# Kernel optimization log

Measured on AMD Instinct MI355X. Metric: run time of the kernel, lower is better.

## Reference

```python
import jax, jax.numpy as jnp
import numpy as np

# ---- constants from the source module ----
NB = [[0,1,2,3],[0,1,4],[0,2,5],[0,3,6],[1,4,7],[2,5,8],[3,6,9],[4,7,10],[5,8,11],[6,9],[7,10],[8,11],[12,13,14,15],[12,13,16],[12,14,17],[12,15],[13,16,18],[14,17,19],[16,18,20],[17,19,21],[18,20,22],[19,21,23],[20,22],[21,23]]
PARENT = np.array([0,0,0,0,1,2,3,4,5,6,7,8,9,9,9,12,13,14,16,17,18,19,20,21])  # root parent sentinel handled separately
KJ, NV, PREG = 24, 6890, 200
LEN = np.array([len(n) for n in NB])
NBR_IDX = np.zeros((KJ,4), np.int32)
NBR_VALID = np.zeros((KJ,4), np.float32)
for k, n in enumerate(NB):
    NBR_IDX[k,:len(n)] = n; NBR_VALID[k,:len(n)] = 1.0
BETA_POS = np.zeros((KJ,17), np.float32); BETA_POS[np.arange(KJ), 4*LEN] = 1.0
SLICE_MASK = np.zeros((23,17), np.float32)
for j in range(23):
    SLICE_MASK[j,:4*LEN[j]+1] = 1.0  # self.K[j] has 4*len(NB[j])+1 rows
NBR_IDX = jnp.asarray(NBR_IDX); NBR_VALID = jnp.asarray(NBR_VALID)
BETA_POS = jnp.asarray(BETA_POS); SLICE_MASK = jnpp = jnp.asarray(SLICE_MASK)


def setup_inputs() -> dict:
    key = jax.random.key(0)
    ks = jax.random.split(key, 9)
    V = jax.random.normal(ks[0], (PREG, NV, 3), jnp.float32)
    T = jax.random.normal(ks[1], (PREG, NV, 3), jnp.float32)
    J = jax.random.normal(ks[2], (PREG, KJ, 3), jnp.float32)
    theta = 0.3 * jax.random.normal(ks[3], (PREG, 72), jnp.float32)
    W_prime = jax.random.uniform(ks[4], (NV, KJ), jnp.float32)
    W_i = jax.random.uniform(ks[5], (NV, KJ), jnp.float32)
    W_i = W_i / W_i.sum(axis=1, keepdims=True)
    A = jax.random.uniform(ks[6], (23, NV), jnp.float32)
    K_mats = 0.01 * jax.random.normal(ks[7], (23, 17, 3 * NV), jnp.float32)
    K_mats = K_mats * SLICE_MASK[:, :, None]  # zero rows beyond the ragged per-joint size
    beta_2 = jnp.ones((1,), jnp.float32)
    return {"V": V, "T": T, "J": J, "theta": theta, "W_prime": W_prime, "W_i": W_i, "A": A, "K_mats": K_mats, "beta_2": beta_2, "epoch": 1}


def _rodrigues(pose):  # pose: (K,3)
    angle = jnp.maximum(jnp.linalg.norm(pose, axis=1, keepdims=True), 1e-8)
    axis = pose / angle
    x, y, z = axis[:, 0], axis[:, 1], axis[:, 2]
    zero = jnp.zeros_like(x)
    skew = jnp.stack([zero, -z, y, z, zero, -x, -y, x, zero], axis=1).reshape(-1, 3, 3)
    outer = axis[:, :, None] * axis[:, None, :]
    c = jnp.cos(angle)[:, :, None]
    s = jnp.sin(angle)[:, :, None]
    eye = jnp.eye(3, dtype=pose.dtype)[None]
    return c * eye + (1.0 - c) * outer + s * skew


def _compute_G(pose72, Jp):  # pose72: (72,), Jp: (K,3) -> (K,4,4)
    R = _rodrigues(pose72.reshape(KJ, 3))
    t = Jp - jnp.concatenate([jnp.zeros((1, 3), Jp.dtype), Jp[PARENT[1:]]], axis=0)
    G_local = jnp.zeros((KJ, 4, 4), Jp.dtype)
    G_local = G_local.at[:, :3, :3].set(R).at[:, :3, 3].set(t).at[:, 3, 3].set(1.0)
    Gs = [G_local[0]]
    for i in range(1, KJ):  # fixed 24-joint kinematic tree
        Gs.append(Gs[PARENT[i]] @ G_local[i])
    G = jnp.stack(Gs, axis=0)
    off = jnp.einsum('kij,kj->ki', G[:, :3, :3], Jp)  # homogeneous w=0 -> rotation only
    return G.at[:, :3, 3].add(-off)


def _axis2quat(p):  # (M,3) -> (M,4)
    angle = jnp.sqrt(jnp.maximum(jnp.sum(p ** 2, axis=1), 1e-16))
    n = p / angle[:, None]
    s = jnp.sin(angle / 2)
    return jnp.stack([n[:, 0] * s, n[:, 1] * s, n[:, 2] * s, jnp.cos(angle / 2) - 1.0], axis=1)


def reference(V, T, J, theta, W_prime, W_i, A, K_mats, beta_2, epoch):
    P = V.shape[0]
    b2 = beta_2[0]
    # normalized skinning weights
    W_relu = jax.nn.relu(W_prime)
    W_change = W_relu / (W_relu.sum(axis=1, keepdims=True) + 1e-8)
    # per-pose global joint transforms
    G_prime = jax.vmap(_compute_G)(theta, J)  # (P,K,4,4)
    # quaternion features and blend-shape correction
    q = _axis2quat(theta.reshape(P * KJ, 3)).reshape(P, KJ, 4)
    qg = q[:, NBR_IDX, :] * NBR_VALID[None, :, :, None]       # (P,K,4,4) neighbor gather
    q17 = jnp.concatenate([qg.reshape(P, KJ, 16), jnp.zeros((P, KJ, 1), q.dtype)], axis=-1)
    q17 = q17 + BETA_POS[None] * b2                            # beta_2 at column 4*len
    qm = q17[:, 1:, :] * SLICE_MASK[None]                      # ragged slice q_ne[:, j+1, :lenK]
    contrib = jnp.einsum('pjl,jlm->pjm', qm, K_mats).reshape(P, 23, NV, 3)
    T_p = jnp.einsum('pjnc,jn->pnc', contrib, jax.nn.relu(A)) + T
    # linear blend skinning
    T_h = jnp.concatenate([T_p, jnp.ones((P, NV, 1), T_p.dtype)], axis=-1)
    transformed = jnp.einsum('pkij,pnj->pnki', G_prime[:, :, :3, :], T_h)  # (P,N,K,3)
    verts = jnp.einsum('nk,pnkc->pnc', W_change, transformed)
    # energies
    e = float(epoch)
    g_wi = 0.1 * np.exp(-0.1 * e)
    g_w = 0.002 * np.exp(-0.008 * e)
    g_a = 0.001 * np.exp(-0.008 * e)
    g_k = 0.1 * np.exp(-0.008 * e)
    E_D = jnp.sum((V - verts) ** 2)
    E_Wi = jnp.sum((W_change - W_i) ** 2)
    E_W = jnp.sum(jnp.abs(W_change))
    E_A = jnp.sum(jnp.abs(A))
    E_K = jnp.sum(jnp.sqrt(jnp.sum(K_mats ** 2, axis=(1, 2))))
    E = E_D + g_wi * E_Wi + g_w * E_W + g_a * E_A + g_k * E_K
    return (E, verts)
```

## Files before the change

### kernel.cpp

```cpp
#include <hip/hip_runtime.h>
#include <math.h>

#define KJ 24
#define NV 6890
#define PREG 200
#define M_TOT (NV*3)
#define KDIM 391
#define KPAD 416
#define TP_STRIDE 20672
#define NMT64 323
#define NSTAGE (NMT64*13)
#define NMT32 646

#define EDP_OFF 0
#define EKP_OFF 5400
#define WIP_OFF 101984
#define EWP_OFF 102016
#define EAP_OFF 102048
#define RED_OFF 102080
#define G_OFF   102112
#define TP_OFF  159712
#define QBH_OFF_U 10903488
#define QBL_OFF_U 11009984
#define BTH_OFF_U 11116480
#define BTL_OFF_U 19716032
#define TP2_OFF 14157792

typedef __attribute__((ext_vector_type(8))) short short8;
typedef __attribute__((ext_vector_type(4))) float f32x4;
typedef __attribute__((ext_vector_type(4))) unsigned int u32x4;

__constant__ int c_PARENT[24] = {0,0,0,0,1,2,3,4,5,6,7,8,9,9,9,12,13,14,16,17,18,19,20,21};
__constant__ int c_DEPTH[24]  = {0,1,1,1,2,2,2,3,3,3,4,4,4,4,4,5,5,5,6,6,7,7,8,8};
__constant__ int c_LEN[24]    = {4,3,3,3,3,3,3,3,3,2,2,2,4,3,3,2,3,3,3,3,3,3,2,2};
__constant__ int c_NBR[24][4] = {
  {0,1,2,3},{0,1,4,0},{0,2,5,0},{0,3,6,0},{1,4,7,0},{2,5,8,0},{3,6,9,0},{4,7,10,0},
  {5,8,11,0},{6,9,0,0},{7,10,0,0},{8,11,0,0},{12,13,14,15},{12,13,16,0},{12,14,17,0},
  {12,15,0,0},{13,16,18,0},{14,17,19,0},{16,18,20,0},{17,19,21,0},{18,20,22,0},
  {19,21,23,0},{20,22,0,0},{21,23,0,0}};

__device__ __forceinline__ float waveReduce(float v) {
  #pragma unroll
  for (int off = 32; off > 0; off >>= 1) v += __shfl_down(v, off, 64);
  return v;
}
__device__ __forceinline__ unsigned short f2bf(float x) {
  union { float f; unsigned u; } v; v.f = x;
  unsigned r = v.u + 0x7FFFu + ((v.u >> 16) & 1u);
  return (unsigned short)(r >> 16);
}
__device__ __forceinline__ float bf2f(unsigned short h) {
  union { unsigned u; float f; } v; v.u = ((unsigned)h) << 16; return v.f;
}

__global__ __launch_bounds__(256) void kPre(const float* __restrict__ J,
                                            const float* __restrict__ theta,
                                            const float* __restrict__ beta2,
                                            const float* __restrict__ Wp,
                                            const float* __restrict__ Wi,
                                            const float* __restrict__ A,
                                            const float* __restrict__ K,
                                            float* __restrict__ ws) {
  unsigned short* qbh = (unsigned short*)ws + QBH_OFF_U;
  unsigned short* qbl = (unsigned short*)ws + QBL_OFF_U;
  int b = blockIdx.x;
  if (b < 50) {
    __shared__ float Gl[4][24][12];
    __shared__ float Gg[4][24][12];
    __shared__ float q[4][24][4];
    int w = threadIdx.x >> 6, t = threadIdx.x & 63;
    int p = b*4 + w;
    if (t < 24) {
      float x = theta[p*72 + 3*t + 0];
      float y = theta[p*72 + 3*t + 1];
      float z = theta[p*72 + 3*t + 2];
      float n2 = x*x + y*y + z*z;
      float ang = fmaxf(sqrtf(n2), 1e-8f);
      float ia = 1.f/ang;
      float ax = x*ia, ay = y*ia, az = z*ia;
      float c = cosf(ang), s = sinf(ang), C = 1.f - c;
      float jx = J[p*72+3*t], jy = J[p*72+3*t+1], jz = J[p*72+3*t+2];
      float tx = jx, ty = jy, tz = jz;
      if (t > 0) {
        int par = c_PARENT[t];
        tx -= J[p*72+3*par]; ty -= J[p*72+3*par+1]; tz -= J[p*72+3*par+2];
      }
      Gl[w][t][0]=c+C*ax*ax;   Gl[w][t][1]=C*ax*ay-s*az; Gl[w][t][2]=C*ax*az+s*ay; Gl[w][t][3]=tx;
      Gl[w][t][4]=C*ax*ay+s*az;Gl[w][t][5]=c+C*ay*ay;    Gl[w][t][6]=C*ay*az-s*ax; Gl[w][t][7]=ty;
      Gl[w][t][8]=C*ax*az-s*ay;Gl[w][t][9]=C*ay*az+s*ax; Gl[w][t][10]=c+C*az*az;   Gl[w][t][11]=tz;
      float ang2 = sqrtf(fmaxf(n2, 1e-16f));
      float inv2 = 1.f/ang2;
      float s2 = sinf(0.5f*ang2);
      q[w][t][0] = x*inv2*s2; q[w][t][1] = y*inv2*s2; q[w][t][2] = z*inv2*s2;
      q[w][t][3] = cosf(0.5f*ang2) - 1.f;
    }
    __syncthreads();
    for (int lev = 0; lev <= 8; lev++) {
      if (t < 24 && c_DEPTH[t] == lev) {
        if (lev == 0) {
          for (int i2 = 0; i2 < 12; i2++) Gg[w][0][i2] = Gl[w][0][i2];
        } else {
          int par = c_PARENT[t];
          for (int r = 0; r < 3; r++) {
            float g0 = Gg[w][par][r*4+0], g1 = Gg[w][par][r*4+1];
            float g2 = Gg[w][par][r*4+2], g3 = Gg[w][par][r*4+3];
            for (int c2 = 0; c2 < 4; c2++) {
              float v = g0*Gl[w][t][0+c2] + g1*Gl[w][t][4+c2] + g2*Gl[w][t][8+c2];
              if (c2 == 3) v += g3;
              Gg[w][t][r*4+c2] = v;
            }
          }
        }
      }
      __syncthreads();
    }
    if (t < 24) {
      float jx = J[p*72+3*t], jy = J[p*72+3*t+1], jz = J[p*72+3*t+2];
      float* gp = ws + G_OFF + p*288 + t*12;
      #pragma unroll
      for (int r = 0; r < 3; r++) {
        float off = Gg[w][t][r*4+0]*jx + Gg[w][t][r*4+1]*jy + Gg[w][t][r*4+2]*jz;
        Gg[w][t][r*4+3] -= off;
      }
      #pragma unroll
      for (int i2 = 0; i2 < 12; i2++) gp[i2] = Gg[w][t][i2];
    }
    __syncthreads();
    float b2 = beta2[0];
    for (int e = t; e < KDIM; e += 64) {
      int j = e / 17, l = e - 17*j;
      int k = j + 1;
      float val = 0.f;
      if (l < 4*c_LEN[j] + 1) {
        if (l < 16) {
          int sidx = l >> 2, cc = l & 3;
          if (sidx < c_LEN[k]) val = q[w][c_NBR[k][sidx]][cc];
        }
        if (l == 4*c_LEN[k]) val += b2;
      }
      unsigned short hi = f2bf(val);
      unsigned short lo = f2bf(val - bf2f(hi));
      qbh[p*KPAD + e] = hi;
      qbl[p*KPAD + e] = lo;
    }
    for (int e = KDIM + t; e < KPAD; e += 64) {
      qbh[p*KPAD + e] = 0; qbl[p*KPAD + e] = 0;
    }
  } else if (b < 77) {
    int d = b - 50;
    int t = threadIdx.x;
    int n = d*256 + t;
    float ewi = 0.f, ew = 0.f, ea = 0.f;
    if (n < NV) {
      float wv[24]; float sum = 0.f;
      const float4* wp4 = (const float4*)(Wp + n*24);
      #pragma unroll
      for (int i = 0; i < 6; i++) {
        float4 v4 = wp4[i];
        wv[4*i+0] = fmaxf(v4.x, 0.f); wv[4*i+1] = fmaxf(v4.y, 0.f);
        wv[4*i+2] = fmaxf(v4.z, 0.f); wv[4*i+3] = fmaxf(v4.w, 0.f);
        sum += wv[4*i+0]+wv[4*i+1]+wv[4*i+2]+wv[4*i+3];
      }
      float inv = 1.f/(sum + 1e-8f);
      #pragma unroll
      for (int k = 0; k < 24; k++) {
        float wc = wv[k]*inv;
        ew += fabsf(wc);
        float dd = wc - Wi[n*24+k];
        ewi += dd*dd;
      }
    }
    for (int i = d*256 + t; i < 23*NV; i += 27*256) ea += fabsf(A[i]);
    for (int i = d*256 + t; i < 56*KPAD; i += 27*256) {
      qbh[200*KPAD + i] = 0; qbl[200*KPAD + i] = 0;
    }
    __shared__ float red[3][4];
    int lane = t & 63, wv2 = t >> 6;
    ewi = waveReduce(ewi); ew = waveReduce(ew); ea = waveReduce(ea);
    if (lane == 0) { red[0][wv2] = ewi; red[1][wv2] = ew; red[2][wv2] = ea; }
    __syncthreads();
    if (t == 0) {
      ws[WIP_OFF + d] = red[0][0]+red[0][1]+red[0][2]+red[0][3];
      ws[EWP_OFF + d] = red[1][0]+red[1][1]+red[1][2]+red[1][3];
      ws[EAP_OFF + d] = red[2][0]+red[2][1]+red[2][2]+red[2][3];
    }
  } else {
    int flat = b - 77;
    int bx = flat % NMT64, by = flat / NMT64;
    int m0 = bx*64, kg0 = by*32;
    __shared__ unsigned short Sh[32*66];
    __shared__ unsigned short Sl[32*66];
    __shared__ float ek[23];
    int t = threadIdx.x;
    if (t < 23) ek[t] = 0.f;
    __syncthreads();
    int krow = t >> 3, mseg = (t & 7) * 8;
    int kg = kg0 + krow;
    int mm = m0 + mseg;
    float kv[8], wv[8]; float sq = 0.f;
    #pragma unroll
    for (int i = 0; i < 8; i++) { kv[i] = 0.f; wv[i] = 0.f; }
    if (kg < KDIM) {
      const float* kr = K + (size_t)kg*M_TOT + mm;
      if (mm + 7 < M_TOT) {
        float4 a4 = *(const float4*)kr; float4 b4 = *(const float4*)(kr+4);
        kv[0]=a4.x; kv[1]=a4.y; kv[2]=a4.z; kv[3]=a4.w;
        kv[4]=b4.x; kv[5]=b4.y; kv[6]=b4.z; kv[7]=b4.w;
      } else {
        #pragma unroll
        for (int i = 0; i < 8; i++) if (mm+i < M_TOT) kv[i] = kr[i];
      }
      int j = kg / 17;
      int nb = mm / 3;
      float av[4];
      #pragma unroll
      for (int i = 0; i < 4; i++)
        av[i] = (nb + i < NV) ? fmaxf(A[j*NV + nb + i], 0.f) : 0.f;
      #pragma unroll
      for (int i = 0; i < 8; i++) {
        float a = (mm+i < M_TOT) ? av[(mm+i)/3 - nb] : 0.f;
        wv[i] = kv[i]*a;
        sq = fmaf(kv[i], kv[i], sq);
      }
    }
    #pragma unroll
    for (int c = 0; c < 4; c++) {
      unsigned short h0 = f2bf(wv[2*c]),  h1 = f2bf(wv[2*c+1]);
      unsigned short l0 = f2bf(wv[2*c]   - bf2f(h0));
      unsigned short l1 = f2bf(wv[2*c+1] - bf2f(h1));
      *(unsigned*)&Sh[krow*66 + mseg + 2*c] = (unsigned)h0 | ((unsigned)h1 << 16);
      *(unsigned*)&Sl[krow*66 + mseg + 2*c] = (unsigned)l0 | ((unsigned)l1 << 16);
    }
    sq += __shfl_xor(sq, 1, 64);
    sq += __shfl_xor(sq, 2, 64);
    sq += __shfl_xor(sq, 4, 64);
    if ((t & 7) == 0 && kg < KDIM) atomicAdd(&ek[kg/17], sq);
    __syncthreads();
    int mrow = t >> 2, kq = t & 3;
    unsigned dh[4], dl[4];
    #pragma unroll
    for (int c2 = 0; c2 < 4; c2++) {
      unsigned short s0 = Sh[(kq*8 + 2*c2    )*66 + mrow];
      unsigned short s1 = Sh[(kq*8 + 2*c2 + 1)*66 + mrow];
      dh[c2] = (unsigned)s0 | ((unsigned)s1 << 16);
      unsigned short u0 = Sl[(kq*8 + 2*c2    )*66 + mrow];
      unsigned short u1 = Sl[(kq*8 + 2*c2 + 1)*66 + mrow];
      dl[c2] = (unsigned)u0 | ((unsigned)u1 << 16);
    }
    unsigned short* BtH = (unsigned short*)ws + BTH_OFF_U;
    unsigned short* BtL = (unsigned short*)ws + BTL_OFF_U;
    size_t o = (size_t)(m0 + mrow)*KPAD + kg0 + kq*8;
    *(u32x4*)(BtH + o) = (u32x4){dh[0], dh[1], dh[2], dh[3]};
    *(u32x4*)(BtL + o) = (u32x4){dl[0], dl[1], dl[2], dl[3]};
    if (t < 23) ws[EKP_OFF + t*NSTAGE + flat] = ek[t];
  }
}

template<int KS0, int NKS>
__device__ __forceinline__ void kb_body(const unsigned short* __restrict__ qbh,
                                        const unsigned short* __restrict__ qbl,
                                        const unsigned short* __restrict__ BtH,
                                        const unsigned short* __restrict__ BtL,
                                        float* __restrict__ TPd, int m0) {
  const int tid = threadIdx.x;
  const int w = tid >> 6, lane = tid & 63;
  const int r = lane & 15, qd = lane >> 4;

  f32x4 acc[4][2];
  #pragma unroll
  for (int h = 0; h < 4; h++)
    #pragma unroll
    for (int f = 0; f < 2; f++) acc[h][f] = (f32x4){0.f,0.f,0.f,0.f};

  int aofs[4], bofs[2];
  #pragma unroll
  for (int h = 0; h < 4; h++) aofs[h] = (w*64 + h*16 + r)*KPAD + qd*8 + KS0*32;
  #pragma unroll
  for (int f = 0; f < 2; f++) bofs[f] = (m0 + f*16 + r)*KPAD + qd*8 + KS0*32;

  short8 ah[2][4], al[2][4], bh[2][2], bl[2][2];
  #pragma unroll
  for (int h = 0; h < 4; h++) {
    ah[0][h] = *(const short8*)(qbh + aofs[h]);
    al[0][h] = *(const short8*)(qbl + aofs[h]);
  }
  #pragma unroll
  for (int f = 0; f < 2; f++) {
    bh[0][f] = *(const short8*)(BtH + bofs[f]);
    bl[0][f] = *(const short8*)(BtL + bofs[f]);
  }
  #pragma unroll
  for (int ks = 0; ks < NKS; ks++) {
    const int cur = ks & 1, nxt = cur ^ 1;
    if (ks + 1 < NKS) {
      const int o = (ks+1)*32;
      #pragma unroll
      for (int h = 0; h < 4; h++) {
        ah[nxt][h] = *(const short8*)(qbh + aofs[h] + o);
        al[nxt][h] = *(const short8*)(qbl + aofs[h] + o);
      }
      #pragma unroll
      for (int f = 0; f < 2; f++) {
        bh[nxt][f] = *(const short8*)(BtH + bofs[f] + o);
        bl[nxt][f] = *(const short8*)(BtL + bofs[f] + o);
      }
    }
    #pragma unroll
    for (int f = 0; f < 2; f++)
      #pragma unroll
      for (int h = 0; h < 4; h++) {
        acc[h][f] = __builtin_amdgcn_mfma_f32_16x16x32_bf16(ah[cur][h], bh[cur][f], acc[h][f], 0, 0, 0);
        acc[h][f] = __builtin_amdgcn_mfma_f32_16x16x32_bf16(ah[cur][h], bl[cur][f], acc[h][f], 0, 0, 0);
        acc[h][f] = __builtin_amdgcn_mfma_f32_16x16x32_bf16(al[cur][h], bh[cur][f], acc[h][f], 0, 0, 0);
      }
  }
  #pragma unroll
  for (int h = 0; h < 4; h++)
    #pragma unroll
    for (int f = 0; f < 2; f++)
      #pragma unroll
      for (int g = 0; g < 4; g++) {
        int p = w*64 + h*16 + qd*4 + g;
        if (p < PREG)
          TPd[(size_t)p*TP_STRIDE + m0 + f*16 + r] = acc[h][f][g];
      }
}

__global__ __launch_bounds__(256) void kB(float* __restrict__ ws) {
  const unsigned short* qbh = (const unsigned short*)ws + QBH_OFF_U;
  const unsigned short* qbl = (const unsigned short*)ws + QBL_OFF_U;
  const unsigned short* BtH = (const unsigned short*)ws + BTH_OFF_U;
  const unsigned short* BtL = (const unsigned short*)ws + BTL_OFF_U;
  const int m0 = blockIdx.x * 32;
  if (blockIdx.y == 0)
    kb_body<0, 7>(qbh, qbl, BtH, BtL, ws + TP_OFF, m0);
  else
    kb_body<7, 6>(qbh, qbl, BtH, BtL, ws + TP2_OFF, m0);
}

__global__ __launch_bounds__(256) void kC(const float* __restrict__ V,
                                          const float* __restrict__ T,
                                          const float* __restrict__ Wp,
                                          const float* __restrict__ ws,
                                          float* __restrict__ out) {
  int p = blockIdx.y;
  int n = blockIdx.x*256 + threadIdx.x;
  const float* __restrict__ gp = ws + G_OFF + (size_t)p*288;
  __shared__ float tmp[4];
  float ed = 0.f;
  if (n < NV) {
    float wv[24]; float sum = 0.f;
    const float4* wp4 = (const float4*)(Wp + n*24);
    #pragma unroll
    for (int i = 0; i < 6; i++) {
      float4 v4 = wp4[i];
      wv[4*i+0] = fmaxf(v4.x, 0.f); wv[4*i+1] = fmaxf(v4.y, 0.f);
      wv[4*i+2] = fmaxf(v4.z, 0.f); wv[4*i+3] = fmaxf(v4.w, 0.f);
      sum += wv[4*i+0]+wv[4*i+1]+wv[4*i+2]+wv[4*i+3];
    }
    float inv = 1.f/(sum + 1e-8f);
    float M[12];
    #pragma unroll
    for (int i = 0; i < 12; i++) M[i] = 0.f;
    #pragma unroll
    for (int k = 0; k < 24; k++) {
      float wc = wv[k];
      #pragma unroll
      for (int i = 0; i < 12; i++)
        M[i] = fmaf(wc, gp[k*12 + i], M[i]);
    }
    #pragma unroll
    for (int i = 0; i < 12; i++) M[i] *= inv;
    size_t tb = (size_t)p*M_TOT + 3*n;
    size_t pb = (size_t)p*TP_STRIDE + 3*n;
    float t0 = ws[TP_OFF + pb + 0] + ws[TP2_OFF + pb + 0] + T[tb + 0];
    float t1 = ws[TP_OFF + pb + 1] + ws[TP2_OFF + pb + 1] + T[tb + 1];
    float t2 = ws[TP_OFF + pb + 2] + ws[TP2_OFF + pb + 2] + T[tb + 2];
    float v0 = M[0]*t0 + M[1]*t1 + M[2]*t2  + M[3];
    float v1 = M[4]*t0 + M[5]*t1 + M[6]*t2  + M[7];
    float v2 = M[8]*t0 + M[9]*t1 + M[10]*t2 + M[11];
    out[1+tb+0] = v0; out[1+tb+1] = v1; out[1+tb+2] = v2;
    float d0 = V[tb+0]-v0, d1 = V[tb+1]-v1, d2 = V[tb+2]-v2;
    ed = d0*d0 + d1*d1 + d2*d2;
  }
  ed = waveReduce(ed);
  int lane = threadIdx.x & 63, w = threadIdx.x >> 6;
  if (lane == 0) tmp[w] = ed;
  __syncthreads();
  if (threadIdx.x == 0)
    ((float*)ws)[EDP_OFF + blockIdx.y*27 + blockIdx.x] = tmp[0]+tmp[1]+tmp[2]+tmp[3];
}

__global__ __launch_bounds__(256) void kF1(float* __restrict__ ws) {
  __shared__ float sb[4];
  int b = blockIdx.x, t = threadIdx.x, lane = t & 63, w = t >> 6;
  if (b < 23) {
    float s = 0.f;
    for (int i = t; i < NSTAGE; i += 256) s += ws[EKP_OFF + b*NSTAGE + i];
    s = waveReduce(s);
    if (lane == 0) sb[w] = s;
    __syncthreads();
    if (t == 0) ws[RED_OFF + b] = sb[0]+sb[1]+sb[2]+sb[3];
  } else if (b == 23) {
    float s = 0.f;
    for (int i = t; i < 5400; i += 256) s += ws[EDP_OFF + i];
    s = waveReduce(s);
    if (lane == 0) sb[w] = s;
    __syncthreads();
    if (t == 0) ws[RED_OFF + 23] = sb[0]+sb[1]+sb[2]+sb[3];
  } else {
    if (w == 0) {
      float s = (lane < 27) ? ws[WIP_OFF + lane] : 0.f;
      s = waveReduce(s);
      if (lane == 0) ws[RED_OFF + 24] = s;
    } else if (w == 1) {
      float s = (lane < 27) ? ws[EWP_OFF + lane] : 0.f;
      s = waveReduce(s);
      if (lane == 0) ws[RED_OFF + 25] = s;
    } else if (w == 2) {
      float s = (lane < 27) ? ws[EAP_OFF + lane] : 0.f;
      s = waveReduce(s);
      if (lane == 0) ws[RED_OFF + 26] = s;
    }
  }
}

__global__ void kF2(const int* __restrict__ epoch, const float* __restrict__ ws,
                    float* __restrict__ out) {
  int t = threadIdx.x;
  float s = (t < 23) ? sqrtf(ws[RED_OFF + t]) : 0.f;
  s = waveReduce(s);
  if (t == 0) {
    float e    = (float)epoch[0];
    float g_wi = 0.1f   * expf(-0.1f  * e);
    float g_w  = 0.002f * expf(-0.008f* e);
    float g_a  = 0.001f * expf(-0.008f* e);
    float g_k  = 0.1f   * expf(-0.008f* e);
    out[0] = ws[RED_OFF+23] + g_wi*ws[RED_OFF+24] + g_w*ws[RED_OFF+25]
           + g_a*ws[RED_OFF+26] + g_k*s;
  }
}

extern "C" void kernel_launch(void* const* d_in, const int* in_sizes, int n_in,
                              void* d_out, int out_size, void* d_ws, size_t ws_size,
                              hipStream_t stream) {
  const float* V     = (const float*)d_in[0];
  const float* T     = (const float*)d_in[1];
  const float* J     = (const float*)d_in[2];
  const float* theta = (const float*)d_in[3];
  const float* Wp    = (const float*)d_in[4];
  const float* Wi    = (const float*)d_in[5];
  const float* A     = (const float*)d_in[6];
  const float* K     = (const float*)d_in[7];
  const float* b2    = (const float*)d_in[8];
  const int*   epoch = (const int*)d_in[9];
  float* out = (float*)d_out;
  float* ws  = (float*)d_ws;

  hipLaunchKernelGGL(kPre, dim3(77 + NSTAGE), dim3(256), 0, stream,
                     J, theta, b2, Wp, Wi, A, K, ws);
  hipLaunchKernelGGL(kB,   dim3(NMT32, 2),    dim3(256), 0, stream, ws);
  hipLaunchKernelGGL(kC,   dim3(27, PREG),    dim3(256), 0, stream, V, T, Wp, ws, out);
  hipLaunchKernelGGL(kF1,  dim3(25),          dim3(256), 0, stream, ws);
  hipLaunchKernelGGL(kF2,  dim3(1),           dim3(64),  0, stream, epoch, ws, out);
}
```

Baseline: 195.4 us.

## Widen kB GEMM tile to 64 columns and stage B operand through LDS

The split-bf16 GEMM kernel kB now covers 64 output columns per block instead of 32, halving the grid. The B operand (BtH/BtL) is loaded cooperatively once per block into double-buffered shared memory and read from there by all four waves, instead of each wave fetching it from global memory itself. This is meant to cut redundant global/L2 traffic for B and to amortise the A-operand loads over twice as many columns. In exchange it adds a __syncthreads per k-step, doubles the accumulator registers, and halves the number of blocks, which could reduce occupancy and latency hiding.

Measured after the change: 182.2 us. 1.07x faster.

```diff
diff --git a/kernel.cpp b/kernel.cpp
--- a/kernel.cpp
+++ b/kernel.cpp
@@ -10,7 +10,6 @@
 #define TP_STRIDE 20672
 #define NMT64 323
 #define NSTAGE (NMT64*13)
-#define NMT32 646
 
 #define EDP_OFF 0
 #define EKP_OFF 5400
@@ -261,63 +260,85 @@
                                         const unsigned short* __restrict__ qbl,
                                         const unsigned short* __restrict__ BtH,
                                         const unsigned short* __restrict__ BtL,
+                                        short (*__restrict__ SBh)[64*40],
+                                        short (*__restrict__ SBl)[64*40],
                                         float* __restrict__ TPd, int m0) {
   const int tid = threadIdx.x;
   const int w = tid >> 6, lane = tid & 63;
   const int r = lane & 15, qd = lane >> 4;
 
-  f32x4 acc[4][2];
+  f32x4 acc[4][4];
   #pragma unroll
   for (int h = 0; h < 4; h++)
     #pragma unroll
-    for (int f = 0; f < 2; f++) acc[h][f] = (f32x4){0.f,0.f,0.f,0.f};
-
-  int aofs[4], bofs[2];
-  #pragma unroll
-  for (int h = 0; h < 4; h++) aofs[h] = (w*64 + h*16 + r)*KPAD + qd*8 + KS0*32;
-  #pragma unroll
-  for (int f = 0; f < 2; f++) bofs[f] = (m0 + f*16 + r)*KPAD + qd*8 + KS0*32;
-
-  short8 ah[2][4], al[2][4], bh[2][2], bl[2][2];
+    for (int f = 0; f < 4; f++) acc[h][f] = (f32x4){0.f,0.f,0.f,0.f};
+
+  int aofs[4];
+  #pragma unroll
+  for (int h = 0; h < 4; h++) aofs[h] = (w*64 + h*16 + r)*KPAD + KS0*32 + qd*8;
+
+  const int srow = tid >> 2, sseg = tid & 3;
+  const size_t gB = (size_t)(m0 + srow)*KPAD + KS0*32 + sseg*8;
+  const int swr = srow*40 + sseg*8;
+
+  short8 ah[2][4], al[2][4];
+  short8 bsh[2], bsl[2];
+
+  bsh[0] = *(const short8*)(BtH + gB);
+  bsl[0] = *(const short8*)(BtL + gB);
   #pragma unroll
   for (int h = 0; h < 4; h++) {
     ah[0][h] = *(const short8*)(qbh + aofs[h]);
     al[0][h] = *(const short8*)(qbl + aofs[h]);
   }
-  #pragma unroll
-  for (int f = 0; f < 2; f++) {
-    bh[0][f] = *(const short8*)(BtH + bofs[f]);
-    bl[0][f] = *(const short8*)(BtL + bofs[f]);
-  }
+  *(short8*)&SBh[0][swr] = bsh[0];
+  *(short8*)&SBl[0][swr] = bsl[0];
+  bsh[1] = *(const short8*)(BtH + gB + 32);
+  bsl[1] = *(const short8*)(BtL + gB + 32);
+  #pragma unroll
+  for (int h = 0; h < 4; h++) {
+    ah[1][h] = *(const short8*)(qbh + aofs[h] + 32);
+    al[1][h] = *(const short8*)(qbl + aofs[h] + 32);
+  }
+  __syncthreads();
+
   #pragma unroll
   for (int ks = 0; ks < NKS; ks++) {
     const int cur = ks & 1, nxt = cur ^ 1;
+    short8 bfh[4], bfl[4];
+    #pragma unroll
+    for (int f = 0; f < 4; f++) {
+      bfh[f] = *(const short8*)&SBh[cur][(f*16 + r)*40 + qd*8];
+      bfl[f] = *(const short8*)&SBl[cur][(f*16 + r)*40 + qd*8];
+    }
+    #pragma unroll
+    for (int f = 0; f < 4; f++)
+      #pragma unroll
+      for (int h = 0; h < 4; h++) {
+        acc[h][f] = __builtin_amdgcn_mfma_f32_16x16x32_bf16(ah[cur][h], bfh[f], acc[h][f], 0, 0, 0);
+        acc[h][f] = __builtin_amdgcn_mfma_f32_16x16x32_bf16(ah[cur][h], bfl[f], acc[h][f], 0, 0, 0);
+        acc[h][f] = __builtin_amdgcn_mfma_f32_16x16x32_bf16(al[cur][h], bfh[f], acc[h][f], 0, 0, 0);
+      }
     if (ks + 1 < NKS) {
-      const int o = (ks+1)*32;
+      *(short8*)&SBh[nxt][swr] = bsh[nxt];
+      *(short8*)&SBl[nxt][swr] = bsl[nxt];
+    }
+    if (ks + 2 < NKS) {
+      const int o = (ks + 2) * 32;
+      bsh[cur] = *(const short8*)(BtH + gB + o);
+      bsl[cur] = *(const short8*)(BtL + gB + o);
       #pragma unroll
       for (int h = 0; h < 4; h++) {
-        ah[nxt][h] = *(const short8*)(qbh + aofs[h] + o);
-        al[nxt][h] = *(const short8*)(qbl + aofs[h] + o);
-      }
-      #pragma unroll
-      for (int f = 0; f < 2; f++) {
-        bh[nxt][f] = *(const short8*)(BtH + bofs[f] + o);
-        bl[nxt][f] = *(const short8*)(BtL + bofs[f] + o);
-      }
-    }
-    #pragma unroll
-    for (int f = 0; f < 2; f++)
-      #pragma unroll
-      for (int h = 0; h < 4; h++) {
-        acc[h][f] = __builtin_amdgcn_mfma_f32_16x16x32_bf16(ah[cur][h], bh[cur][f], acc[h][f], 0, 0, 0);
-        acc[h][f] = __builtin_amdgcn_mfma_f32_16x16x32_bf16(ah[cur][h], bl[cur][f], acc[h][f], 0, 0, 0);
-        acc[h][f] = __builtin_amdgcn_mfma_f32_16x16x32_bf16(al[cur][h], bh[cur][f], acc[h][f], 0, 0, 0);
-      }
+        ah[cur][h] = *(const short8*)(qbh + aofs[h] + o);
+        al[cur][h] = *(const short8*)(qbl + aofs[h] + o);
+      }
+    }
+    __syncthreads();
   }
   #pragma unroll
   for (int h = 0; h < 4; h++)
     #pragma unroll
-    for (int f = 0; f < 2; f++)
+    for (int f = 0; f < 4; f++)
       #pragma unroll
       for (int g = 0; g < 4; g++) {
         int p = w*64 + h*16 + qd*4 + g;
@@ -327,15 +348,17 @@
 }
 
 __global__ __launch_bounds__(256) void kB(float* __restrict__ ws) {
+  __shared__ short SBh[2][64*40];
+  __shared__ short SBl[2][64*40];
   const unsigned short* qbh = (const unsigned short*)ws + QBH_OFF_U;
   const unsigned short* qbl = (const unsigned short*)ws + QBL_OFF_U;
   const unsigned short* BtH = (const unsigned short*)ws + BTH_OFF_U;
   const unsigned short* BtL = (const unsigned short*)ws + BTL_OFF_U;
-  const int m0 = blockIdx.x * 32;
+  const int m0 = blockIdx.x * 64;
   if (blockIdx.y == 0)
-    kb_body<0, 7>(qbh, qbl, BtH, BtL, ws + TP_OFF, m0);
+    kb_body<0, 7>(qbh, qbl, BtH, BtL, SBh, SBl, ws + TP_OFF, m0);
   else
-    kb_body<7, 6>(qbh, qbl, BtH, BtL, ws + TP2_OFF, m0);
+    kb_body<7, 6>(qbh, qbl, BtH, BtL, SBh, SBl, ws + TP2_OFF, m0);
 }
 
 __global__ __launch_bounds__(256) void kC(const float* __restrict__ V,
@@ -459,7 +482,7 @@
 
   hipLaunchKernelGGL(kPre, dim3(77 + NSTAGE), dim3(256), 0, stream,
                      J, theta, b2, Wp, Wi, A, K, ws);
-  hipLaunchKernelGGL(kB,   dim3(NMT32, 2),    dim3(256), 0, stream, ws);
+  hipLaunchKernelGGL(kB,   dim3(NMT64, 2),    dim3(256), 0, stream, ws);
   hipLaunchKernelGGL(kC,   dim3(27, PREG),    dim3(256), 0, stream, V, T, Wp, ws, out);
   hipLaunchKernelGGL(kF1,  dim3(25),          dim3(256), 0, stream, ws);
   hipLaunchKernelGGL(kF2,  dim3(1),           dim3(64),  0, stream, epoch, ws, out);
```
